# Performance work log

Measured on AMD Instinct MI355X. Metric: run time of the kernel, lower is better.

The kernel has to match this reference:

```python
import jax, jax.numpy as jnp
import numpy as np
import math

B, S, HID = 2, 1024, 2048
NH, HD = 16, 128
STREAM_R, SELECT_R, RECENT_R = 0.02, 0.06, 0.08
FF = 0.9  # forgetting factor
ROPE_BASE = 10000.0


def setup_inputs() -> dict:
    key = jax.random.key(0)
    ks = jax.random.split(key, 5)
    return {
        "hidden_states": jax.random.normal(ks[0], (B, S, HID), dtype=jnp.float32),
        "wq": jax.random.normal(ks[1], (HID, HID), dtype=jnp.float32) * 0.02,
        "wk": jax.random.normal(ks[2], (HID, HID), dtype=jnp.float32) * 0.02,
        "wv": jax.random.normal(ks[3], (HID, HID), dtype=jnp.float32) * 0.02,
        "wo": jax.random.normal(ks[4], (HID, HID), dtype=jnp.float32) * 0.02,
    }


def _rope_tables(seq_len, dim):
    inv_freq = 1.0 / (ROPE_BASE ** (jnp.arange(0, dim, 2, dtype=jnp.float32) / dim))
    freqs = jnp.outer(jnp.arange(seq_len, dtype=jnp.float32), inv_freq)  # [S, D/2]
    emb = jnp.concatenate([freqs, freqs], axis=-1)  # [S, D]
    return jnp.cos(emb), jnp.sin(emb)


def _rotate_half(x):
    x1, x2 = jnp.split(x, 2, axis=-1)
    return jnp.concatenate([-x2, x1], axis=-1)


def a2s_base_mask(attn_weights, sb, selb, rb, ff):
    # attn_weights: [B,H,S,S] (causal mask already added). Returns bool keep-mask [B,H,S,S].
    Bv, Hv, Sq, Sk = attn_weights.shape
    scores = jax.nn.softmax(attn_weights.astype(jnp.float32), axis=-1)  # [B,H,S,S]
    cb = sb + selb + rb  # cache budget
    # EMA warmup over first cb rows: sum_i ff^(cb-1-i) * scores[i]
    w = ff ** jnp.arange(cb - 1, -1, -1, dtype=jnp.float32)
    select0 = jnp.einsum('t,bhts->bhs', w, scores[:, :, :cb, :])
    mask0 = jnp.ones((Bv, Hv, Sk), dtype=bool)
    pos = jnp.arange(Sk)

    xs_scores = jnp.moveaxis(scores[:, :, cb:Sk - 1, :], 2, 0)  # [T,B,H,S]
    ts = jnp.arange(cb, Sk - 1, dtype=jnp.int32)

    def step(carry, inp):
        sel, m = carry
        sc, t = inp
        cur = sc * m
        cur = cur / jnp.sum(cur, axis=-1, keepdims=True)
        sel = ff * sel + cur
        local = t - rb
        # argmin over window [sb : local+1]; outside -> +inf (evicted entries already +inf)
        win = jnp.where((pos >= sb) & (pos <= local), sel, jnp.inf)
        mi = jnp.argmin(win, axis=-1)  # [B,H], first-min like torch
        evict = pos == mi[..., None]  # [B,H,S] one-hot bool
        sel = jnp.where(evict, jnp.inf, sel)
        m_new = m & ~evict
        return (sel, m_new), m_new

    _, rows = jax.lax.scan(step, (select0, mask0), (xs_scores, ts))
    head = jnp.ones((Bv, Hv, cb + 1, Sk), dtype=bool)  # rows 0..cb stay all-True
    tail = jnp.moveaxis(rows, 0, 2)  # rows cb+1..S-1
    return jnp.concatenate([head, tail], axis=2)


def reference(hidden_states, wq, wk, wv, wo):
    sb = math.floor(STREAM_R * S + 0.5)
    selb = math.floor(SELECT_R * S + 0.5)
    rb = math.floor(RECENT_R * S + 0.5)

    q = (hidden_states @ wq).reshape(B, S, NH, HD).transpose(0, 2, 1, 3)
    k = (hidden_states @ wk).reshape(B, S, NH, HD).transpose(0, 2, 1, 3)
    v = (hidden_states @ wv).reshape(B, S, NH, HD).transpose(0, 2, 1, 3)

    cos, sin = _rope_tables(S, HD)  # [S,HD]
    q = q * cos + _rotate_half(q) * sin
    k = k * cos + _rotate_half(k) * sin

    attn = jnp.einsum('bhqd,bhkd->bhqk', q, k) / math.sqrt(HD)
    mask_val = jnp.finfo(jnp.float32).min
    causal = jnp.where(jnp.tril(jnp.ones((S, S), dtype=bool)), 0.0, mask_val)[None, None]
    attn = jnp.maximum(attn + causal, mask_val)

    keep = a2s_base_mask(jax.lax.stop_gradient(attn), sb, selb, rb, FF)
    attn = jnp.where(keep, attn, mask_val)  # torch.min(attention_mask) == mask_val

    probs = jax.nn.softmax(attn.astype(jnp.float32), axis=-1).astype(q.dtype)
    out = jnp.einsum('bhqk,bhkd->bhqd', probs, v)
    out = out.transpose(0, 2, 1, 3).reshape(B, S, HID)
    return out @ wo
```

## Files before the change

### kernel.cpp

```cpp
#include <hip/hip_runtime.h>
#include <math.h>

#define Bb    2
#define Ss    1024
#define HIDd  2048
#define NHh   16
#define HDd   128
#define SBc   20
#define SELBc 61
#define RBc   82
#define CBc   163
#define FFf   0.9f
#define MASKVAL (-3.4028234663852886e38f)
#define NBH   (Bb*NHh)
#define NROWS (NBH*Ss)

typedef __attribute__((ext_vector_type(8))) short short8;
typedef __attribute__((ext_vector_type(4))) float f32x4;

__device__ __forceinline__ unsigned short f2b(float f) {
    unsigned u = __float_as_uint(f);
    u = (u + 0x7FFFu + ((u >> 16) & 1u)) >> 16;
    return (unsigned short)u;
}
__device__ __forceinline__ float b2f(unsigned short h) {
    return __uint_as_float((unsigned)h << 16);
}

__global__ __launch_bounds__(256) void conv_split(const float* __restrict__ x,
                                                  unsigned short* __restrict__ yh,
                                                  unsigned short* __restrict__ yl, int n4)
{
    int i = blockIdx.x * 256 + threadIdx.x;
    if (i >= n4) return;
    float4 v = ((const float4*)x)[i];
    ushort4 h, l;
    h.x = f2b(v.x); l.x = f2b(v.x - b2f(h.x));
    h.y = f2b(v.y); l.y = f2b(v.y - b2f(h.y));
    h.z = f2b(v.z); l.z = f2b(v.z - b2f(h.z));
    h.w = f2b(v.w); l.w = f2b(v.w - b2f(h.w));
    ((ushort4*)yh)[i] = h;
    ((ushort4*)yl)[i] = l;
}

__global__ __launch_bounds__(256) void tconv(const float* __restrict__ W,
                                             unsigned short* __restrict__ Wt,
                                             int Kdim, int Ndim)
{
    __shared__ float T[64][65];
    int n0 = blockIdx.x * 64, k0 = blockIdx.y * 64;
    int tid = threadIdx.x;
    int rr = tid >> 4, cc = (tid & 15) * 4;
#pragma unroll
    for (int p = 0; p < 4; ++p) {
        int r = rr + p * 16;
        float4 x = *(const float4*)&W[(size_t)(k0 + r) * Ndim + n0 + cc];
        T[r][cc] = x.x; T[r][cc + 1] = x.y; T[r][cc + 2] = x.z; T[r][cc + 3] = x.w;
    }
    __syncthreads();
#pragma unroll
    for (int p = 0; p < 4; ++p) {
        int rn = rr + p * 16;
        ushort4 o;
        o.x = f2b(T[cc][rn]);     o.y = f2b(T[cc + 1][rn]);
        o.z = f2b(T[cc + 2][rn]); o.w = f2b(T[cc + 3][rn]);
        *(ushort4*)&Wt[(size_t)(n0 + rn) * Kdim + k0 + cc] = o;
    }
}

__global__ __launch_bounds__(256) void tconv_split(const float* __restrict__ W,
                                                   unsigned short* __restrict__ Wth,
                                                   unsigned short* __restrict__ Wtl,
                                                   int Kdim, int Ndim)
{
    __shared__ float T[64][65];
    int n0 = blockIdx.x * 64, k0 = blockIdx.y * 64;
    int tid = threadIdx.x;
    int rr = tid >> 4, cc = (tid & 15) * 4;
#pragma unroll
    for (int p = 0; p < 4; ++p) {
        int r = rr + p * 16;
        float4 x = *(const float4*)&W[(size_t)(k0 + r) * Ndim + n0 + cc];
        T[r][cc] = x.x; T[r][cc + 1] = x.y; T[r][cc + 2] = x.z; T[r][cc + 3] = x.w;
    }
    __syncthreads();
#pragma unroll
    for (int p = 0; p < 4; ++p) {
        int rn = rr + p * 16;
        float v0 = T[cc][rn], v1 = T[cc + 1][rn], v2 = T[cc + 2][rn], v3 = T[cc + 3][rn];
        ushort4 h, l;
        h.x = f2b(v0); l.x = f2b(v0 - b2f(h.x));
        h.y = f2b(v1); l.y = f2b(v1 - b2f(h.y));
        h.z = f2b(v2); l.z = f2b(v2 - b2f(h.z));
        h.w = f2b(v3); l.w = f2b(v3 - b2f(h.w));
        *(ushort4*)&Wth[(size_t)(n0 + rn) * Kdim + k0 + cc] = h;
        *(ushort4*)&Wtl[(size_t)(n0 + rn) * Kdim + k0 + cc] = l;
    }
}

template<int MODE>
__global__ __launch_bounds__(256) void gemm_bf16t(const unsigned short* __restrict__ A,
                                                  const unsigned short* __restrict__ Bt,
                                                  float* __restrict__ C,
                                                  int M, int N, int K)
{
    __shared__ unsigned short As[128 * 32];
    __shared__ unsigned short Bs[128 * 32];
    const int tid = threadIdx.x;
    const int bm = blockIdx.y * 128, bn = blockIdx.x * 128;
    const int lane = tid & 63, wid = tid >> 6;
    const int wr = (wid >> 1) * 64, wc = (wid & 1) * 64;
    const int lm = lane & 15, lk = (lane >> 4) * 8;

    f32x4 acc[4][4];
#pragma unroll
    for (int mi = 0; mi < 4; ++mi)
#pragma unroll
        for (int ni = 0; ni < 4; ++ni) acc[mi][ni] = 0.0f;

    for (int k0 = 0; k0 < K; k0 += 32) {
#pragma unroll
        for (int l = 0; l < 2; ++l) {
            int L = tid + l * 256;
            int row = L >> 2, c8 = (L & 3) * 8;
            *(short8*)&As[row * 32 + c8] = *(const short8*)&A[(size_t)(bm + row) * K + k0 + c8];
            *(short8*)&Bs[row * 32 + c8] = *(const short8*)&Bt[(size_t)(bn + row) * K + k0 + c8];
        }
        __syncthreads();
        short8 af[4], bf[4];
#pragma unroll
        for (int mi = 0; mi < 4; ++mi) af[mi] = *(short8*)&As[(wr + mi * 16 + lm) * 32 + lk];
#pragma unroll
        for (int ni = 0; ni < 4; ++ni) bf[ni] = *(short8*)&Bs[(wc + ni * 16 + lm) * 32 + lk];
#pragma unroll
        for (int mi = 0; mi < 4; ++mi)
#pragma unroll
            for (int ni = 0; ni < 4; ++ni)
                acc[mi][ni] = __builtin_amdgcn_mfma_f32_16x16x32_bf16(af[mi], bf[ni], acc[mi][ni], 0, 0, 0);
        __syncthreads();
    }
    const int lr = (lane >> 4) * 4;
#pragma unroll
    for (int mi = 0; mi < 4; ++mi)
#pragma unroll
        for (int ni = 0; ni < 4; ++ni)
#pragma unroll
            for (int r = 0; r < 4; ++r) {
                int m = bm + wr + mi * 16 + lr + r;
                int n = bn + wc + ni * 16 + lm;
                float vv = acc[mi][ni][r];
                if (MODE == 0) {
                    C[(size_t)m * N + n] = vv;
                } else {
                    int b_ = m / Ss, s_ = m % Ss;
                    int h_ = n / HDd, d_ = n % HDd;
                    C[(size_t)((b_ * NHh + h_) * Ss + s_) * HDd + d_] = vv;
                }
            }
}

template<int MODE>
__global__ __launch_bounds__(256) void gemm_split(const unsigned short* __restrict__ Ah,
                                                  const unsigned short* __restrict__ Al,
                                                  const unsigned short* __restrict__ Bh,
                                                  const unsigned short* __restrict__ Bl,
                                                  float* __restrict__ C,
                                                  int M, int N, int K)
{
    __shared__ unsigned short AsH[128 * 32], AsL[128 * 32];
    __shared__ unsigned short BsH[128 * 32], BsL[128 * 32];
    const int tid = threadIdx.x;
    const int bm = blockIdx.y * 128, bn = blockIdx.x * 128;
    const int lane = tid & 63, wid = tid >> 6;
    const int wr = (wid >> 1) * 64, wc = (wid & 1) * 64;
    const int lm = lane & 15, lk = (lane >> 4) * 8;

    f32x4 acc[4][4];
#pragma unroll
    for (int mi = 0; mi < 4; ++mi)
#pragma unroll
        for (int ni = 0; ni < 4; ++ni) acc[mi][ni] = 0.0f;

    for (int k0 = 0; k0 < K; k0 += 32) {
#pragma unroll
        for (int l = 0; l < 2; ++l) {
            int L = tid + l * 256;
            int row = L >> 2, c8 = (L & 3) * 8;
            size_t ga = (size_t)(bm + row) * K + k0 + c8;
            size_t gb = (size_t)(bn + row) * K + k0 + c8;
            *(short8*)&AsH[row * 32 + c8] = *(const short8*)&Ah[ga];
            *(short8*)&AsL[row * 32 + c8] = *(const short8*)&Al[ga];
            *(short8*)&BsH[row * 32 + c8] = *(const short8*)&Bh[gb];
            *(short8*)&BsL[row * 32 + c8] = *(const short8*)&Bl[gb];
        }
        __syncthreads();
        short8 ah[4], al[4], bh[4], bl[4];
#pragma unroll
        for (int mi = 0; mi < 4; ++mi) {
            ah[mi] = *(short8*)&AsH[(wr + mi * 16 + lm) * 32 + lk];
            al[mi] = *(short8*)&AsL[(wr + mi * 16 + lm) * 32 + lk];
        }
#pragma unroll
        for (int ni = 0; ni < 4; ++ni) {
            bh[ni] = *(short8*)&BsH[(wc + ni * 16 + lm) * 32 + lk];
            bl[ni] = *(short8*)&BsL[(wc + ni * 16 + lm) * 32 + lk];
        }
#pragma unroll
        for (int mi = 0; mi < 4; ++mi)
#pragma unroll
            for (int ni = 0; ni < 4; ++ni) {
                acc[mi][ni] = __builtin_amdgcn_mfma_f32_16x16x32_bf16(ah[mi], bh[ni], acc[mi][ni], 0, 0, 0);
                acc[mi][ni] = __builtin_amdgcn_mfma_f32_16x16x32_bf16(ah[mi], bl[ni], acc[mi][ni], 0, 0, 0);
                acc[mi][ni] = __builtin_amdgcn_mfma_f32_16x16x32_bf16(al[mi], bh[ni], acc[mi][ni], 0, 0, 0);
            }
        __syncthreads();
    }
    const int lr = (lane >> 4) * 4;
#pragma unroll
    for (int mi = 0; mi < 4; ++mi)
#pragma unroll
        for (int ni = 0; ni < 4; ++ni)
#pragma unroll
            for (int r = 0; r < 4; ++r) {
                int m = bm + wr + mi * 16 + lr + r;
                int n = bn + wc + ni * 16 + lm;
                float vv = acc[mi][ni][r];
                if (MODE == 0) {
                    C[(size_t)m * N + n] = vv;
                } else {
                    int b_ = m / Ss, s_ = m % Ss;
                    int h_ = n / HDd, d_ = n % HDd;
                    C[(size_t)((b_ * NHh + h_) * Ss + s_) * HDd + d_] = vv;
                }
            }
}

__global__ __launch_bounds__(64) void rope_qk_split(const float* __restrict__ q,
                                                    const float* __restrict__ k,
                                                    unsigned short* __restrict__ qh,
                                                    unsigned short* __restrict__ ql,
                                                    unsigned short* __restrict__ kh,
                                                    unsigned short* __restrict__ kl)
{
    int idx = blockIdx.x;
    int s = idx % Ss;
    int d = threadIdx.x;
    float inv = powf(10000.0f, -2.0f * (float)d / 128.0f);
    float fr = (float)s * inv;
    float c = cosf(fr), sn = sinf(fr);
    size_t base = (size_t)idx * HDd;
    float q1 = q[base + d], q2 = q[base + d + 64];
    float k1 = k[base + d], k2 = k[base + d + 64];
    float qa = q1 * c - q2 * sn, qbv = q2 * c + q1 * sn;
    float ka = k1 * c - k2 * sn, kbv = k2 * c + k1 * sn;
    unsigned short h;
    h = f2b(qa);  qh[base + d]      = h; ql[base + d]      = f2b(qa  - b2f(h));
    h = f2b(qbv); qh[base + d + 64] = h; ql[base + d + 64] = f2b(qbv - b2f(h));
    h = f2b(ka);  kh[base + d]      = h; kl[base + d]      = f2b(ka  - b2f(h));
    h = f2b(kbv); kh[base + d + 64] = h; kl[base + d + 64] = f2b(kbv - b2f(h));
}

__global__ __launch_bounds__(256) void attn_qk_split(const unsigned short* __restrict__ qh,
                                                     const unsigned short* __restrict__ ql,
                                                     const unsigned short* __restrict__ kh,
                                                     const unsigned short* __restrict__ kl,
                                                     float* __restrict__ attn)
{
    const int bh = blockIdx.z;
    const int bm = blockIdx.y * 128, bn = blockIdx.x * 128;
    float* C = attn + (size_t)bh * Ss * Ss;
    const int tid = threadIdx.x;

    if (blockIdx.x > blockIdx.y) {
        float4 mv = make_float4(MASKVAL, MASKVAL, MASKVAL, MASKVAL);
#pragma unroll
        for (int i = 0; i < 16; ++i) {
            int L = tid + i * 256;
            int row = L >> 5, c4 = (L & 31) * 4;
            *(float4*)&C[(size_t)(bm + row) * Ss + bn + c4] = mv;
        }
        return;
    }
    const size_t hb = (size_t)bh * Ss * HDd;
    const unsigned short* Ah = qh + hb;
    const unsigned short* Al = ql + hb;
    const unsigned short* Bh = kh + hb;
    const unsigned short* Bl = kl + hb;

    __shared__ unsigned short AsH[128 * 32], AsL[128 * 32];
    __shared__ unsigned short BsH[128 * 32], BsL[128 * 32];
    const int lane = tid & 63, wid = tid >> 6;
    const int wr = (wid >> 1) * 64, wc = (wid & 1) * 64;
    const int lm = lane & 15, lk = (lane >> 4) * 8;

    f32x4 acc[4][4];
#pragma unroll
    for (int mi = 0; mi < 4; ++mi)
#pragma unroll
        for (int ni = 0; ni < 4; ++ni) acc[mi][ni] = 0.0f;

    for (int k0 = 0; k0 < HDd; k0 += 32) {
#pragma unroll
        for (int l = 0; l < 2; ++l) {
            int L = tid + l * 256;
            int row = L >> 2, c8 = (L & 3) * 8;
            size_t ga = (size_t)(bm + row) * HDd + k0 + c8;
            size_t gb = (size_t)(bn + row) * HDd + k0 + c8;
            *(short8*)&AsH[row * 32 + c8] = *(const short8*)&Ah[ga];
            *(short8*)&AsL[row * 32 + c8] = *(const short8*)&Al[ga];
            *(short8*)&BsH[row * 32 + c8] = *(const short8*)&Bh[gb];
            *(short8*)&BsL[row * 32 + c8] = *(const short8*)&Bl[gb];
        }
        __syncthreads();
        short8 ah[4], al[4], bh2[4], bl2[4];
#pragma unroll
        for (int mi = 0; mi < 4; ++mi) {
            ah[mi] = *(short8*)&AsH[(wr + mi * 16 + lm) * 32 + lk];
            al[mi] = *(short8*)&AsL[(wr + mi * 16 + lm) * 32 + lk];
        }
#pragma unroll
        for (int ni = 0; ni < 4; ++ni) {
            bh2[ni] = *(short8*)&BsH[(wc + ni * 16 + lm) * 32 + lk];
            bl2[ni] = *(short8*)&BsL[(wc + ni * 16 + lm) * 32 + lk];
        }
#pragma unroll
        for (int mi = 0; mi < 4; ++mi)
#pragma unroll
            for (int ni = 0; ni < 4; ++ni) {
                acc[mi][ni] = __builtin_amdgcn_mfma_f32_16x16x32_bf16(ah[mi], bh2[ni], acc[mi][ni], 0, 0, 0);
                acc[mi][ni] = __builtin_amdgcn_mfma_f32_16x16x32_bf16(ah[mi], bl2[ni], acc[mi][ni], 0, 0, 0);
                acc[mi][ni] = __builtin_amdgcn_mfma_f32_16x16x32_bf16(al[mi], bh2[ni], acc[mi][ni], 0, 0, 0);
            }
        __syncthreads();
    }
    const float scale = 0.08838834764831845f;
    const int lr = (lane >> 4) * 4;
#pragma unroll
    for (int mi = 0; mi < 4; ++mi)
#pragma unroll
        for (int ni = 0; ni < 4; ++ni)
#pragma unroll
            for (int r = 0; r < 4; ++r) {
                int sq = bm + wr + mi * 16 + lr + r;
                int sk = bn + wc + ni * 16 + lm;
                C[(size_t)sq * Ss + sk] = (sk <= sq) ? acc[mi][ni][r] * scale : MASKVAL;
            }
}

__global__ __launch_bounds__(256) void softmax_rows(float* __restrict__ attn)
{
    int row = blockIdx.x;
    float4* a4 = (float4*)(attn + (size_t)row * Ss);
    int tid = threadIdx.x;
    float4 x = a4[tid];
    float m = fmaxf(fmaxf(x.x, x.y), fmaxf(x.z, x.w));
#pragma unroll
    for (int off = 32; off; off >>= 1) m = fmaxf(m, __shfl_xor(m, off));
    __shared__ float red[4];
    if ((tid & 63) == 0) red[tid >> 6] = m;
    __syncthreads();
    float mm = fmaxf(fmaxf(red[0], red[1]), fmaxf(red[2], red[3]));
    float e0 = expf(x.x - mm), e1 = expf(x.y - mm);
    float e2 = expf(x.z - mm), e3 = expf(x.w - mm);
    float s = e0 + e1 + e2 + e3;
#pragma unroll
    for (int off = 32; off; off >>= 1) s += __shfl_xor(s, off);
    __shared__ float red2[4];
    if ((tid & 63) == 0) red2[tid >> 6] = s;
    __syncthreads();
    float inv = 1.0f / (red2[0] + red2[1] + red2[2] + red2[3]);
    a4[tid] = make_float4(e0 * inv, e1 * inv, e2 * inv, e3 * inv);
}

template<int CTRL>
__device__ __forceinline__ int dpp_i(int x) {
    return __builtin_amdgcn_update_dpp(0, x, CTRL, 0xF, 0xF, true);
}
__device__ __forceinline__ float wave_sum64(float x) {
    x += __int_as_float(dpp_i<0xB1>(__float_as_int(x)));
    x += __int_as_float(dpp_i<0x4E>(__float_as_int(x)));
    x += __int_as_float(dpp_i<0x141>(__float_as_int(x)));
    x += __int_as_float(dpp_i<0x140>(__float_as_int(x)));
    int xi = __float_as_int(x);
    float a = __int_as_float(__builtin_amdgcn_readlane(xi, 0));
    float b = __int_as_float(__builtin_amdgcn_readlane(xi, 16));
    float c = __int_as_float(__builtin_amdgcn_readlane(xi, 32));
    float d = __int_as_float(__builtin_amdgcn_readlane(xi, 48));
    return (a + c) + (b + d);
}

__device__ __forceinline__ unsigned long long u64min(unsigned long long a, unsigned long long b) {
    return a < b ? a : b;
}
template<int CTRL>
__device__ __forceinline__ unsigned long long dpp64(unsigned long long x) {
    int lo = (int)(unsigned)x;
    int hi = (int)(unsigned)(x >> 32);
    unsigned l2 = (unsigned)dpp_i<CTRL>(lo);
    unsigned h2 = (unsigned)dpp_i<CTRL>(hi);
    return ((unsigned long long)h2 << 32) | (unsigned long long)l2;
}
__device__ __forceinline__ unsigned long long wave_min64k(unsigned long long x) {
    x = u64min(x, dpp64<0xB1>(x));
    x = u64min(x, dpp64<0x4E>(x));
    x = u64min(x, dpp64<0x141>(x));
    x = u64min(x, dpp64<0x140>(x));
    int lo = (int)(unsigned)x;
    int hi = (int)(unsigned)(x >> 32);
    unsigned long long a = ((unsigned long long)(unsigned)__builtin_amdgcn_readlane(hi, 0)  << 32) |
                           (unsigned long long)(unsigned)__builtin_amdgcn_readlane(lo, 0);
    unsigned long long b = ((unsigned long long)(unsigned)__builtin_amdgcn_readlane(hi, 16) << 32) |
                           (unsigned long long)(unsigned)__builtin_amdgcn_readlane(lo, 16);
    unsigned long long c = ((unsigned long long)(unsigned)__builtin_amdgcn_readlane(hi, 32) << 32) |
                           (unsigned long long)(unsigned)__builtin_amdgcn_readlane(lo, 32);
    unsigned long long d = ((unsigned long long)(unsigned)__builtin_amdgcn_readlane(hi, 48) << 32) |
                           (unsigned long long)(unsigned)__builtin_amdgcn_readlane(lo, 48);
    return u64min(u64min(a, b), u64min(c, d));
}

__device__ __forceinline__ float f4c(float4 v, int i) {
    return i == 0 ? v.x : (i == 1 ? v.y : (i == 2 ? v.z : v.w));
}

template<int NC, int NCL>
__device__ __forceinline__ void scan_step(int t, int lane,
                                          const float4* __restrict__ A4,
                                          unsigned char* __restrict__ KP,
                                          float4 (&rb)[4],
                                          float (&sel)[4][4],
                                          float (&mf)[4][4])
{
    const float INFv = __int_as_float(0x7f800000);
    float4 a[NC];
#pragma unroll
    for (int jj = 0; jj < NC; ++jj) a[jj] = rb[jj];
    int tp = t + 4; if (tp > Ss - 1) tp = Ss - 1;
#pragma unroll
    for (int jj = 0; jj < NCL; ++jj) rb[jj] = A4[tp * 256 + jj * 64 + lane];

    float lsum = 0.0f;
#pragma unroll
    for (int jj = 0; jj < NC; ++jj) {
        float c0 = a[jj].x * mf[jj][0], c1 = a[jj].y * mf[jj][1];
        float c2 = a[jj].z * mf[jj][2], c3 = a[jj].w * mf[jj][3];
        lsum += (c0 + c1) + (c2 + c3);
    }
    float tot = wave_sum64(lsum);
    float inv = 1.0f / tot;

    const int local = t - RBc;
    const int base = lane * 4;
    const bool ge = (base >= SBc);

    unsigned long long kmin = 0xFFFFFFFFFFFFFFFFull;
#pragma unroll
    for (int jj = 0; jj < NC; ++jj) {
        unsigned long long kk[4];
#pragma unroll
        for (int i = 0; i < 4; ++i) {
            float sv = fmaf(FFf, sel[jj][i], f4c(a[jj], i) * inv);
            sel[jj][i] = sv;
            int s = jj * 256 + base + i;
            bool win = (s <= local) && (jj > 0 || ge);
            unsigned hi = win ? __float_as_uint(sv) : 0x7f800000u;
            kk[i] = ((unsigned long long)hi << 32) | (unsigned long long)(unsigned)s;
        }
        unsigned long long cm = u64min(u64min(kk[0], kk[1]), u64min(kk[2], kk[3]));
        kmin = u64min(kmin, cm);
    }
    kmin = wave_min64k(kmin);
    const int besti = (int)(unsigned)(kmin & 0xFFFFFFFFull);

#pragma unroll
    for (int jj = 0; jj < NC; ++jj)
#pragma unroll
        for (int i = 0; i < 4; ++i) {
            int s = jj * 256 + base + i;
            bool e = (s == besti);
            sel[jj][i] = e ? INFv : sel[jj][i];
            mf[jj][i]  = e ? 0.0f : mf[jj][i];
        }

    uchar4* kp4 = (uchar4*)(KP + (size_t)(t + 1) * Ss);
#pragma unroll
    for (int jj = 0; jj < NC; ++jj) {
        uchar4 kb;
        kb.x = (unsigned char)mf[jj][0];
        kb.y = (unsigned char)mf[jj][1];
        kb.z = (unsigned char)mf[jj][2];
        kb.w = (unsigned char)mf[jj][3];
        kp4[jj * 64 + lane] = kb;
    }
}

__global__ __launch_bounds__(64) void scan_kernel5(const float* __restrict__ scores,
                                                   unsigned char* __restrict__ keep)
{
    int bh = blockIdx.x;
    int lane = threadIdx.x;
    const float4* A4 = (const float4*)(scores + (size_t)bh * Ss * Ss);
    unsigned char* KP = keep + (size_t)bh * Ss * Ss;

    float sel[4][4];
    float mf[4][4];
#pragma unroll
    for (int jj = 0; jj < 4; ++jj)
#pragma unroll
        for (int i = 0; i < 4; ++i) { sel[jj][i] = 0.0f; mf[jj][i] = 1.0f; }

    float4 w0 = A4[0 * 256 + lane];
    float4 w1 = A4[1 * 256 + lane];
    float4 w2 = A4[2 * 256 + lane];
    float4 w3 = A4[3 * 256 + lane];
#define WSTEP(W, NEXT)                                                       \
    do {                                                                     \
        float4 _a = W;                                                       \
        W = A4[(NEXT) * 256 + lane];                                         \
        sel[0][0] = fmaf(FFf, sel[0][0], _a.x);                              \
        sel[0][1] = fmaf(FFf, sel[0][1], _a.y);                              \
        sel[0][2] = fmaf(FFf, sel[0][2], _a.z);                              \
        sel[0][3] = fmaf(FFf, sel[0][3], _a.w);                              \
    } while (0)
    for (int r = 0; r < 160; r += 4) {
        WSTEP(w0, r + 4); WSTEP(w1, r + 5); WSTEP(w2, r + 6); WSTEP(w3, r + 7);
    }
#undef WSTEP
    {
        float4 tl[3] = { w0, w1, w2 };
#pragma unroll
        for (int u = 0; u < 3; ++u) {
            sel[0][0] = fmaf(FFf, sel[0][0], tl[u].x);
            sel[0][1] = fmaf(FFf, sel[0][1], tl[u].y);
            sel[0][2] = fmaf(FFf, sel[0][2], tl[u].z);
            sel[0][3] = fmaf(FFf, sel[0][3], tl[u].w);
        }
    }

    float4 rb[4][4];
#pragma unroll
    for (int slot = 0; slot < 4; ++slot)
        rb[slot][0] = A4[(163 + slot) * 256 + lane];

    for (int t0 = 163; t0 < 255; t0 += 4) {
        scan_step<1, 2>(t0 + 0, lane, A4, KP, rb[0], sel, mf);
        scan_step<1, 2>(t0 + 1, lane, A4, KP, rb[1], sel, mf);
        scan_step<1, 2>(t0 + 2, lane, A4, KP, rb[2], sel, mf);
        scan_step<1, 2>(t0 + 3, lane, A4, KP, rb[3], sel, mf);
    }
    for (int t0 = 255; t0 < 511; t0 += 4) {
        scan_step<2, 3>(t0 + 0, lane, A4, KP, rb[0], sel, mf);
        scan_step<2, 3>(t0 + 1, lane, A4, KP, rb[1], sel, mf);
        scan_step<2, 3>(t0 + 2, lane, A4, KP, rb[2], sel, mf);
        scan_step<2, 3>(t0 + 3, lane, A4, KP, rb[3], sel, mf);
    }
    for (int t0 = 511; t0 < 767; t0 += 4) {
        scan_step<3, 4>(t0 + 0, lane, A4, KP, rb[0], sel, mf);
        scan_step<3, 4>(t0 + 1, lane, A4, KP, rb[1], sel, mf);
        scan_step<3, 4>(t0 + 2, lane, A4, KP, rb[2], sel, mf);
        scan_step<3, 4>(t0 + 3, lane, A4, KP, rb[3], sel, mf);
    }
    for (int t0 = 767; t0 < 1023; t0 += 4) {
        scan_step<4, 4>(t0 + 0, lane, A4, KP, rb[0], sel, mf);
        scan_step<4, 4>(t0 + 1, lane, A4, KP, rb[1], sel, mf);
        scan_step<4, 4>(t0 + 2, lane, A4, KP, rb[2], sel, mf);
        scan_step<4, 4>(t0 + 3, lane, A4, KP, rb[3], sel, mf);
    }
}

__global__ __launch_bounds__(256) void renorm_rows(float* __restrict__ scores,
                                                   const unsigned char* __restrict__ keep)
{
    int row = blockIdx.x;
    int r = row % Ss;
    float4* a4 = (float4*)(scores + (size_t)row * Ss);
    int tid = threadIdx.x;
    float4 x = a4[tid];
    if (r > CBc) {
        const uchar4* kp = (const uchar4*)(keep + (size_t)row * Ss);
        uchar4 kb = kp[tid];
        if (!kb.x) x.x = 0.0f;
        if (!kb.y) x.y = 0.0f;
        if (!kb.z) x.z = 0.0f;
        if (!kb.w) x.w = 0.0f;
    }
    float s = (x.x + x.y) + (x.z + x.w);
#pragma unroll
    for (int off = 32; off; off >>= 1) s += __shfl_xor(s, off);
    __shared__ float red2[4];
    if ((tid & 63) == 0) red2[tid >> 6] = s;
    __syncthreads();
    float inv = 1.0f / (red2[0] + red2[1] + red2[2] + red2[3]);
    a4[tid] = make_float4(x.x * inv, x.y * inv, x.z * inv, x.w * inv);
}

__global__ __launch_bounds__(256) void pv_gemm(const float* __restrict__ probs,
                                               const float* __restrict__ v,
                                               unsigned short* __restrict__ ctxb)
{
    int bh = blockIdx.z;
    int b_ = bh / NHh, h_ = bh % NHh;
    const float* P = probs + (size_t)bh * Ss * Ss;
    const float* V = v     + (size_t)bh * Ss * HDd;
    int bm = blockIdx.y * 64, bn = blockIdx.x * 64;
    int tid = threadIdx.x, tx = tid & 15, ty = tid >> 4;
    __shared__ float As[16][65];
    __shared__ float Bs[16][64];
    float acc[4][4] = {};
    int kend = bm + 64;
    for (int k0 = 0; k0 < kend; k0 += 16) {
#pragma unroll
        for (int l = 0; l < 4; ++l) {
            int idx = tid + l * 256;
            int r = idx >> 4, c = idx & 15;
            As[c][r] = P[(size_t)(bm + r) * Ss + k0 + c];
        }
#pragma unroll
        for (int l = 0; l < 4; ++l) {
            int idx = tid + l * 256;
            int r = idx >> 6, c = idx & 63;
            Bs[r][c] = V[(size_t)(k0 + r) * HDd + bn + c];
        }
        __syncthreads();
#pragma unroll
        for (int kk = 0; kk < 16; ++kk) {
            float a[4], b[4];
#pragma unroll
            for (int i = 0; i < 4; ++i) a[i] = As[kk][ty * 4 + i];
#pragma unroll
            for (int j = 0; j < 4; ++j) b[j] = Bs[kk][tx * 4 + j];
#pragma unroll
            for (int i = 0; i < 4; ++i)
#pragma unroll
                for (int j = 0; j < 4; ++j)
                    acc[i][j] = fmaf(a[i], b[j], acc[i][j]);
        }
        __syncthreads();
    }
#pragma unroll
    for (int i = 0; i < 4; ++i) {
        int sq = bm + ty * 4 + i;
#pragma unroll
        for (int j = 0; j < 4; ++j) {
            int d = bn + tx * 4 + j;
            ctxb[(size_t)(b_ * Ss + sq) * HIDd + h_ * HDd + d] = f2b(acc[i][j]);
        }
    }
}

extern "C" void kernel_launch(void* const* d_in, const int* in_sizes, int n_in,
                              void* d_out, int out_size, void* d_ws, size_t ws_size,
                              hipStream_t stream)
{
    const float* hs = (const float*)d_in[0];
    const float* wq = (const float*)d_in[1];
    const float* wk = (const float*)d_in[2];
    const float* wv = (const float*)d_in[3];
    const float* wo = (const float*)d_in[4];
    float* out = (float*)d_out;

    float* ws = (float*)d_ws;
    size_t off = 0;
    float* qf   = ws + off; off += (size_t)NBH * Ss * HDd;
    float* kf   = ws + off; off += (size_t)NBH * Ss * HDd;
    float* vf   = ws + off; off += (size_t)NBH * Ss * HDd;
    float* attn = ws + off; off += (size_t)NBH * Ss * Ss;
    unsigned char* keep = (unsigned char*)(ws + off); off += (size_t)NBH * Ss * Ss / 4;
    unsigned short* wot = (unsigned short*)(ws + off); off += (size_t)HIDd * HIDd / 2;

    unsigned short* hsh  = (unsigned short*)(attn);
    unsigned short* hsl  = (unsigned short*)(attn + 2u * 1024 * 1024);
    unsigned short* wqth = (unsigned short*)(attn + 4u * 1024 * 1024);
    unsigned short* wqtl = (unsigned short*)(attn + 6u * 1024 * 1024);
    unsigned short* wkth = (unsigned short*)(attn + 8u * 1024 * 1024);
    unsigned short* wktl = (unsigned short*)(attn + 10u * 1024 * 1024);
    unsigned short* wvt  = (unsigned short*)(attn + 12u * 1024 * 1024);
    unsigned short* qh = (unsigned short*)keep;
    unsigned short* ql = (unsigned short*)(keep + 8u * 1024 * 1024);
    unsigned short* kh = (unsigned short*)(keep + 16u * 1024 * 1024);
    unsigned short* kl = (unsigned short*)(keep + 24u * 1024 * 1024);
    unsigned short* ctxb = (unsigned short*)qf;

    dim3 blk(256);
    const int M = Bb * Ss;

    conv_split<<<dim3((M * HIDd / 4 + 255) / 256), blk, 0, stream>>>(hs, hsh, hsl, M * HIDd / 4);

    dim3 gt(HIDd / 64, HIDd / 64);
    tconv_split<<<gt, blk, 0, stream>>>(wq, wqth, wqtl, HIDd, HIDd);
    tconv_split<<<gt, blk, 0, stream>>>(wk, wkth, wktl, HIDd, HIDd);
    tconv<<<gt, blk, 0, stream>>>(wv, wvt, HIDd, HIDd);
    tconv<<<gt, blk, 0, stream>>>(wo, wot, HIDd, HIDd);

    dim3 gp(HIDd / 128, M / 128);
    gemm_split<1><<<gp, blk, 0, stream>>>(hsh, hsl, wqth, wqtl, qf, M, HIDd, HIDd);
    gemm_split<1><<<gp, blk, 0, stream>>>(hsh, hsl, wkth, wktl, kf, M, HIDd, HIDd);
    gemm_bf16t<1><<<gp, blk, 0, stream>>>(hsh, wvt, vf, M, HIDd, HIDd);

    rope_qk_split<<<dim3(NBH * Ss), dim3(64), 0, stream>>>(qf, kf, qh, ql, kh, kl);

    attn_qk_split<<<dim3(Ss / 128, Ss / 128, NBH), blk, 0, stream>>>(qh, ql, kh, kl, attn);

    softmax_rows<<<dim3(NROWS), blk, 0, stream>>>(attn);

    scan_kernel5<<<dim3(NBH), dim3(64), 0, stream>>>(attn, keep);

    renorm_rows<<<dim3(NROWS), blk, 0, stream>>>(attn, keep);

    pv_gemm<<<dim3(HDd / 64, Ss / 64, NBH), blk, 0, stream>>>(attn, vf, ctxb);

    gemm_bf16t<0><<<gp, blk, 0, stream>>>(ctxb, wot, out, M, HIDd, HIDd);
}
```

Before: 1.040 ms.

## Fuse mask renorm into PV GEMM, streamline scan argmin, use direct global-to-LDS loads

Three changes land together. The renorm_rows pass is folded into the PV GEMM: masked probabilities are zeroed as they are loaded, row sums are accumulated alongside the FMA loop, and the output is scaled by the inverse sum. This removes a full read and write of the attention matrix. The eviction scan precomputes slot indices, skips window tests for chunks entirely inside the window, and updates only the evicted slot via a uniform broadcast rather than comparing every element. The bf16 GEMM tile loads switch to the global_load_lds builtin when it is available, which also changes the LDS store layout to a linear index.

```diff
diff --git a/kernel.cpp b/kernel.cpp
--- a/kernel.cpp
+++ b/kernel.cpp
@@ -27,6 +27,22 @@
     return __uint_as_float((unsigned)h << 16);
 }
 
+#if defined(__has_builtin)
+#if __has_builtin(__builtin_amdgcn_global_load_lds)
+#define USE_GLD 1
+#endif
+#endif
+
+__device__ __forceinline__ void gload16(const void* g, void* l) {
+#ifdef USE_GLD
+    __builtin_amdgcn_global_load_lds(
+        (const __attribute__((address_space(1))) void*)g,
+        (__attribute__((address_space(3))) void*)l, 16, 0, 0);
+#else
+    *(short8*)l = *(const short8*)g;
+#endif
+}
+
 __global__ __launch_bounds__(256) void conv_split(const float* __restrict__ x,
                                                   unsigned short* __restrict__ yh,
                                                   unsigned short* __restrict__ yl, int n4)
@@ -123,8 +139,8 @@
         for (int l = 0; l < 2; ++l) {
             int L = tid + l * 256;
             int row = L >> 2, c8 = (L & 3) * 8;
-            *(short8*)&As[row * 32 + c8] = *(const short8*)&A[(size_t)(bm + row) * K + k0 + c8];
-            *(short8*)&Bs[row * 32 + c8] = *(const short8*)&Bt[(size_t)(bn + row) * K + k0 + c8];
+            gload16(&A[(size_t)(bm + row) * K + k0 + c8], &As[L * 8]);
+            gload16(&Bt[(size_t)(bn + row) * K + k0 + c8], &Bs[L * 8]);
         }
         __syncthreads();
         short8 af[4], bf[4];
@@ -188,10 +204,10 @@
             int row = L >> 2, c8 = (L & 3) * 8;
             size_t ga = (size_t)(bm + row) * K + k0 + c8;
             size_t gb = (size_t)(bn + row) * K + k0 + c8;
-            *(short8*)&AsH[row * 32 + c8] = *(const short8*)&Ah[ga];
-            *(short8*)&AsL[row * 32 + c8] = *(const short8*)&Al[ga];
-            *(short8*)&BsH[row * 32 + c8] = *(const short8*)&Bh[gb];
-            *(short8*)&BsL[row * 32 + c8] = *(const short8*)&Bl[gb];
+            gload16(&Ah[ga], &AsH[L * 8]);
+            gload16(&Al[ga], &AsL[L * 8]);
+            gload16(&Bh[gb], &BsH[L * 8]);
+            gload16(&Bl[gb], &BsL[L * 8]);
         }
         __syncthreads();
         short8 ah[4], al[4], bh[4], bl[4];
@@ -306,10 +322,10 @@
             int row = L >> 2, c8 = (L & 3) * 8;
             size_t ga = (size_t)(bm + row) * HDd + k0 + c8;
             size_t gb = (size_t)(bn + row) * HDd + k0 + c8;
-            *(short8*)&AsH[row * 32 + c8] = *(const short8*)&Ah[ga];
-            *(short8*)&AsL[row * 32 + c8] = *(const short8*)&Al[ga];
-            *(short8*)&BsH[row * 32 + c8] = *(const short8*)&Bh[gb];
-            *(short8*)&BsL[row * 32 + c8] = *(const short8*)&Bl[gb];
+            gload16(&Ah[ga], &AsH[L * 8]);
+            gload16(&Al[ga], &AsL[L * 8]);
+            gload16(&Bh[gb], &BsH[L * 8]);
+            gload16(&Bl[gb], &BsL[L * 8]);
         }
         __syncthreads();
         short8 ah[4], al[4], bh2[4], bl2[4];
@@ -428,7 +444,9 @@
                                           unsigned char* __restrict__ KP,
                                           float4 (&rb)[4],
                                           float (&sel)[4][4],
-                                          float (&mf)[4][4])
+                                          float (&mf)[4][4],
+                                          const int (&sreg)[4][4],
+                                          bool ge)
 {
     const float INFv = __int_as_float(0x7f800000);
     float4 a[NC];
@@ -449,37 +467,56 @@
     float inv = 1.0f / tot;
 
     const int local = t - RBc;
-    const int base = lane * 4;
-    const bool ge = (base >= SBc);
+    const int lead = local >> 8;
 
     unsigned long long kmin = 0xFFFFFFFFFFFFFFFFull;
 #pragma unroll
     for (int jj = 0; jj < NC; ++jj) {
-        unsigned long long kk[4];
+        float sv[4];
 #pragma unroll
         for (int i = 0; i < 4; ++i) {
-            float sv = fmaf(FFf, sel[jj][i], f4c(a[jj], i) * inv);
-            sel[jj][i] = sv;
-            int s = jj * 256 + base + i;
-            bool win = (s <= local) && (jj > 0 || ge);
-            unsigned hi = win ? __float_as_uint(sv) : 0x7f800000u;
-            kk[i] = ((unsigned long long)hi << 32) | (unsigned long long)(unsigned)s;
-        }
-        unsigned long long cm = u64min(u64min(kk[0], kk[1]), u64min(kk[2], kk[3]));
-        kmin = u64min(kmin, cm);
+            sv[i] = fmaf(FFf, sel[jj][i], f4c(a[jj], i) * inv);
+            sel[jj][i] = sv[i];
+        }
+        if (jj < lead) {
+            unsigned long long kk[4];
+#pragma unroll
+            for (int i = 0; i < 4; ++i) {
+                unsigned hi = __float_as_uint(sv[i]);
+                if (jj == 0) hi = ge ? hi : 0x7f800000u;
+                kk[i] = ((unsigned long long)hi << 32) | (unsigned long long)(unsigned)sreg[jj][i];
+            }
+            kmin = u64min(kmin, u64min(u64min(kk[0], kk[1]), u64min(kk[2], kk[3])));
+        } else if (jj == lead) {
+            unsigned long long kk[4];
+#pragma unroll
+            for (int i = 0; i < 4; ++i) {
+                bool win = (sreg[jj][i] <= local) && (jj > 0 || ge);
+                unsigned hi = win ? __float_as_uint(sv[i]) : 0x7f800000u;
+                kk[i] = ((unsigned long long)hi << 32) | (unsigned long long)(unsigned)sreg[jj][i];
+            }
+            kmin = u64min(kmin, u64min(u64min(kk[0], kk[1]), u64min(kk[2], kk[3])));
+        }
     }
     kmin = wave_min64k(kmin);
-    const int besti = (int)(unsigned)(kmin & 0xFFFFFFFFull);
-
-#pragma unroll
-    for (int jj = 0; jj < NC; ++jj)
-#pragma unroll
-        for (int i = 0; i < 4; ++i) {
-            int s = jj * 256 + base + i;
-            bool e = (s == besti);
-            sel[jj][i] = e ? INFv : sel[jj][i];
-            mf[jj][i]  = e ? 0.0f : mf[jj][i];
-        }
+
+    const int besti  = __builtin_amdgcn_readfirstlane((int)(unsigned)(kmin & 0xFFFFFFFFull));
+    const int echunk = besti >> 8;
+    const int eslot  = besti & 3;
+    const int elane  = (besti >> 2) & 63;
+    const bool lmatch = (lane == elane);
+#pragma unroll
+    for (int jj = 0; jj < NC; ++jj) {
+        if (jj == echunk) {
+#pragma unroll
+            for (int i = 0; i < 4; ++i) {
+                if (i == eslot) {
+                    sel[jj][i] = lmatch ? INFv : sel[jj][i];
+                    mf[jj][i]  = lmatch ? 0.0f : mf[jj][i];
+                }
+            }
+        }
+    }
 
     uchar4* kp4 = (uchar4*)(KP + (size_t)(t + 1) * Ss);
 #pragma unroll
@@ -493,7 +530,7 @@
     }
 }
 
-__global__ __launch_bounds__(64) void scan_kernel5(const float* __restrict__ scores,
+__global__ __launch_bounds__(64) void scan_kernel6(const float* __restrict__ scores,
                                                    unsigned char* __restrict__ keep)
 {
     int bh = blockIdx.x;
@@ -503,10 +540,15 @@
 
     float sel[4][4];
     float mf[4][4];
+    int sreg[4][4];
 #pragma unroll
     for (int jj = 0; jj < 4; ++jj)
 #pragma unroll
-        for (int i = 0; i < 4; ++i) { sel[jj][i] = 0.0f; mf[jj][i] = 1.0f; }
+        for (int i = 0; i < 4; ++i) {
+            sel[jj][i] = 0.0f; mf[jj][i] = 1.0f;
+            sreg[jj][i] = jj * 256 + lane * 4 + i;
+        }
+    const bool ge = (lane * 4 >= SBc);
 
     float4 w0 = A4[0 * 256 + lane];
     float4 w1 = A4[1 * 256 + lane];
@@ -542,77 +584,57 @@
         rb[slot][0] = A4[(163 + slot) * 256 + lane];
 
     for (int t0 = 163; t0 < 255; t0 += 4) {
-        scan_step<1, 2>(t0 + 0, lane, A4, KP, rb[0], sel, mf);
-        scan_step<1, 2>(t0 + 1, lane, A4, KP, rb[1], sel, mf);
-        scan_step<1, 2>(t0 + 2, lane, A4, KP, rb[2], sel, mf);
-        scan_step<1, 2>(t0 + 3, lane, A4, KP, rb[3], sel, mf);
+        scan_step<1, 2>(t0 + 0, lane, A4, KP, rb[0], sel, mf, sreg, ge);
+        scan_step<1, 2>(t0 + 1, lane, A4, KP, rb[1], sel, mf, sreg, ge);
+        scan_step<1, 2>(t0 + 2, lane, A4, KP, rb[2], sel, mf, sreg, ge);
+        scan_step<1, 2>(t0 + 3, lane, A4, KP, rb[3], sel, mf, sreg, ge);
     }
     for (int t0 = 255; t0 < 511; t0 += 4) {
-        scan_step<2, 3>(t0 + 0, lane, A4, KP, rb[0], sel, mf);
-        scan_step<2, 3>(t0 + 1, lane, A4, KP, rb[1], sel, mf);
-        scan_step<2, 3>(t0 + 2, lane, A4, KP, rb[2], sel, mf);
-        scan_step<2, 3>(t0 + 3, lane, A4, KP, rb[3], sel, mf);
+        scan_step<2, 3>(t0 + 0, lane, A4, KP, rb[0], sel, mf, sreg, ge);
+        scan_step<2, 3>(t0 + 1, lane, A4, KP, rb[1], sel, mf, sreg, ge);
+        scan_step<2, 3>(t0 + 2, lane, A4, KP, rb[2], sel, mf, sreg, ge);
+        scan_step<2, 3>(t0 + 3, lane, A4, KP, rb[3], sel, mf, sreg, ge);
     }
     for (int t0 = 511; t0 < 767; t0 += 4) {
-        scan_step<3, 4>(t0 + 0, lane, A4, KP, rb[0], sel, mf);
-        scan_step<3, 4>(t0 + 1, lane, A4, KP, rb[1], sel, mf);
-        scan_step<3, 4>(t0 + 2, lane, A4, KP, rb[2], sel, mf);
-        scan_step<3, 4>(t0 + 3, lane, A4, KP, rb[3], sel, mf);
+        scan_step<3, 4>(t0 + 0, lane, A4, KP, rb[0], sel, mf, sreg, ge);
+        scan_step<3, 4>(t0 + 1, lane, A4, KP, rb[1], sel, mf, sreg, ge);
+        scan_step<3, 4>(t0 + 2, lane, A4, KP, rb[2], sel, mf, sreg, ge);
+        scan_step<3, 4>(t0 + 3, lane, A4, KP, rb[3], sel, mf, sreg, ge);
     }
     for (int t0 = 767; t0 < 1023; t0 += 4) {
-        scan_step<4, 4>(t0 + 0, lane, A4, KP, rb[0], sel, mf);
-        scan_step<4, 4>(t0 + 1, lane, A4, KP, rb[1], sel, mf);
-        scan_step<4, 4>(t0 + 2, lane, A4, KP, rb[2], sel, mf);
-        scan_step<4, 4>(t0 + 3, lane, A4, KP, rb[3], sel, mf);
-    }
-}
-
-__global__ __launch_bounds__(256) void renorm_rows(float* __restrict__ scores,
-                                                   const unsigned char* __restrict__ keep)
-{
-    int row = blockIdx.x;
-    int r = row % Ss;
-    float4* a4 = (float4*)(scores + (size_t)row * Ss);
-    int tid = threadIdx.x;
-    float4 x = a4[tid];
-    if (r > CBc) {
-        const uchar4* kp = (const uchar4*)(keep + (size_t)row * Ss);
-        uchar4 kb = kp[tid];
-        if (!kb.x) x.x = 0.0f;
-        if (!kb.y) x.y = 0.0f;
-        if (!kb.z) x.z = 0.0f;
-        if (!kb.w) x.w = 0.0f;
-    }
-    float s = (x.x + x.y) + (x.z + x.w);
-#pragma unroll
-    for (int off = 32; off; off >>= 1) s += __shfl_xor(s, off);
-    __shared__ float red2[4];
-    if ((tid & 63) == 0) red2[tid >> 6] = s;
-    __syncthreads();
-    float inv = 1.0f / (red2[0] + red2[1] + red2[2] + red2[3]);
-    a4[tid] = make_float4(x.x * inv, x.y * inv, x.z * inv, x.w * inv);
-}
-
-__global__ __launch_bounds__(256) void pv_gemm(const float* __restrict__ probs,
-                                               const float* __restrict__ v,
-                                               unsigned short* __restrict__ ctxb)
+        scan_step<4, 4>(t0 + 0, lane, A4, KP, rb[0], sel, mf, sreg, ge);
+        scan_step<4, 4>(t0 + 1, lane, A4, KP, rb[1], sel, mf, sreg, ge);
+        scan_step<4, 4>(t0 + 2, lane, A4, KP, rb[2], sel, mf, sreg, ge);
+        scan_step<4, 4>(t0 + 3, lane, A4, KP, rb[3], sel, mf, sreg, ge);
+    }
+}
+
+__global__ __launch_bounds__(256) void pv_renorm(const float* __restrict__ scores,
+                                                 const unsigned char* __restrict__ keep,
+                                                 const float* __restrict__ v,
+                                                 unsigned short* __restrict__ ctxb)
 {
     int bh = blockIdx.z;
     int b_ = bh / NHh, h_ = bh % NHh;
-    const float* P = probs + (size_t)bh * Ss * Ss;
-    const float* V = v     + (size_t)bh * Ss * HDd;
+    const float* P = scores + (size_t)bh * Ss * Ss;
+    const unsigned char* KPm = keep + (size_t)bh * Ss * Ss;
+    const float* V = v + (size_t)bh * Ss * HDd;
     int bm = blockIdx.y * 64, bn = blockIdx.x * 64;
     int tid = threadIdx.x, tx = tid & 15, ty = tid >> 4;
     __shared__ float As[16][65];
     __shared__ float Bs[16][64];
     float acc[4][4] = {};
+    float rs[4] = {};
     int kend = bm + 64;
     for (int k0 = 0; k0 < kend; k0 += 16) {
 #pragma unroll
         for (int l = 0; l < 4; ++l) {
             int idx = tid + l * 256;
             int r = idx >> 4, c = idx & 15;
-            As[c][r] = P[(size_t)(bm + r) * Ss + k0 + c];
+            int row = bm + r;
+            float p = P[(size_t)row * Ss + k0 + c];
+            if (row > CBc && !KPm[(size_t)row * Ss + k0 + c]) p = 0.0f;
+            As[c][r] = p;
         }
 #pragma unroll
         for (int l = 0; l < 4; ++l) {
@@ -629,6 +651,8 @@
 #pragma unroll
             for (int j = 0; j < 4; ++j) b[j] = Bs[kk][tx * 4 + j];
 #pragma unroll
+            for (int i = 0; i < 4; ++i) rs[i] += a[i];
+#pragma unroll
             for (int i = 0; i < 4; ++i)
 #pragma unroll
                 for (int j = 0; j < 4; ++j)
@@ -638,11 +662,12 @@
     }
 #pragma unroll
     for (int i = 0; i < 4; ++i) {
+        float inv = 1.0f / rs[i];
         int sq = bm + ty * 4 + i;
 #pragma unroll
         for (int j = 0; j < 4; ++j) {
             int d = bn + tx * 4 + j;
-            ctxb[(size_t)(b_ * Ss + sq) * HIDd + h_ * HDd + d] = f2b(acc[i][j]);
+            ctxb[(size_t)(b_ * Ss + sq) * HIDd + h_ * HDd + d] = f2b(acc[i][j] * inv);
         }
     }
 }
@@ -702,11 +727,9 @@
 
     softmax_rows<<<dim3(NROWS), blk, 0, stream>>>(attn);
 
-    scan_kernel5<<<dim3(NBH), dim3(64), 0, stream>>>(attn, keep);
-
-    renorm_rows<<<dim3(NROWS), blk, 0, stream>>>(attn, keep);
-
-    pv_gemm<<<dim3(HDd / 64, Ss / 64, NBH), blk, 0, stream>>>(attn, vf, ctxb);
+    scan_kernel6<<<dim3(NBH), dim3(64), 0, stream>>>(attn, keep);
+
+    pv_renorm<<<dim3(HDd / 64, Ss / 64, NBH), blk, 0, stream>>>(attn, keep, vf, ctxb);
 
     gemm_bf16t<0><<<gp, blk, 0, stream>>>(ctxb, wot, out, M, HIDd, HIDd);
 }
```

Result: slower. 1.191 ms (+14.5%).
